# Kernel optimization log

Hardware: AMD Instinct MI355X
Metric: run time of the kernel (lower is better)

Reference implementation:

```python
import math
import jax, jax.numpy as jnp
import numpy as np

N, C_S, C_Z, C, H, PQK, PV = 768, 384, 128, 16, 12, 4, 8
INF, EPS = 100000.0, 1e-8


def _quat_to_rot(q):
    # q: [N,4] normalized quaternions -> [N,3,3] rotation matrices
    w, x, y, z = q[:, 0], q[:, 1], q[:, 2], q[:, 3]
    return jnp.stack([
        jnp.stack([1 - 2 * (y * y + z * z), 2 * (x * y - w * z), 2 * (x * z + w * y)], -1),
        jnp.stack([2 * (x * y + w * z), 1 - 2 * (x * x + z * z), 2 * (y * z - w * x)], -1),
        jnp.stack([2 * (x * z - w * y), 2 * (y * z + w * x), 1 - 2 * (x * x + y * y)], -1),
    ], -2)


def setup_inputs() -> dict:
    key = jax.random.key(0)
    ks = jax.random.split(key, 16)
    quat = jax.random.normal(ks[2], (N, 4))
    quat = quat / jnp.linalg.norm(quat, axis=-1, keepdims=True)
    sc = 0.02
    return {
        "s": jax.random.normal(ks[0], (N, C_S), jnp.float32),
        "z": jax.random.normal(ks[1], (N, N, C_Z), jnp.float32),
        "rot": _quat_to_rot(quat).astype(jnp.float32),
        "trans": jax.random.normal(ks[3], (N, 3), jnp.float32),
        "mask": jnp.ones((N,), jnp.float32),
        "Wq": sc * jax.random.normal(ks[4], (C_S, H * C), jnp.float32),
        "bq": jnp.zeros((H * C,), jnp.float32),
        "Wqp": sc * jax.random.normal(ks[5], (C_S, H * 3 * PQK), jnp.float32),
        "bqp": jnp.zeros((H * 3 * PQK,), jnp.float32),
        "Wkv": sc * jax.random.normal(ks[6], (C_S, 2 * H * C), jnp.float32),
        "bkv": jnp.zeros((2 * H * C,), jnp.float32),
        "Wkvp": sc * jax.random.normal(ks[7], (C_S, H * 3 * (PQK + PV)), jnp.float32),
        "bkvp": jnp.zeros((H * 3 * (PQK + PV),), jnp.float32),
        "Wb": sc * jax.random.normal(ks[8], (C_Z, H), jnp.float32),
        "bb": jnp.zeros((H,), jnp.float32),
        "head_weights": 0.5413 * jnp.ones((H,), jnp.float32),  # softplus^{-1}(1)
        "Wout": sc * jax.random.normal(ks[9], (H * (C_Z + C + PV * 4), C_S), jnp.float32),
        "bout": jnp.zeros((C_S,), jnp.float32),
    }


def _proj_points(x, W, b, rot, trans, P):
    # PointProjection: split last dim into 3 coord chunks, stack as last axis
    pl = x @ W + b                                   # [N, H*3*P]
    pl = pl.reshape(-1, 3, H * P).transpose(0, 2, 1).reshape(-1, H, P, 3)
    return jnp.einsum('nij,nhpj->nhpi', rot, pl) + trans[:, None, None, :]


def reference(s, z, rot, trans, mask, Wq, bq, Wqp, bqp, Wkv, bkv, Wkvp, bkvp,
              Wb, bb, head_weights, Wout, bout):
    q = (s @ Wq + bq).reshape(N, H, C)
    kv = (s @ Wkv + bkv).reshape(N, H, 2 * C)
    k, v = kv[..., :C], kv[..., C:]
    q_pts = _proj_points(s, Wqp, bqp, rot, trans, PQK)          # [N,H,PQK,3]
    kv_pts = _proj_points(s, Wkvp, bkvp, rot, trans, PQK + PV)  # [N,H,PQK+PV,3]
    k_pts, v_pts = kv_pts[..., :PQK, :], kv_pts[..., PQK:, :]

    b_bias = z @ Wb + bb                                        # [N,N,H]
    a = jnp.einsum('qhc,khc->hqk', q, k) * math.sqrt(1.0 / (3 * C))
    a = a + math.sqrt(1.0 / 3) * jnp.transpose(b_bias, (2, 0, 1))

    # point-distance attention: [q,k,H,PQK]
    d2 = jnp.sum((q_pts[:, None] - k_pts[None]) ** 2, axis=-1)
    hw = jax.nn.softplus(head_weights) * math.sqrt(1.0 / (3 * (PQK * 9.0 / 2)))
    pt_att = -0.5 * jnp.sum(d2 * hw[:, None], axis=-1)          # [q,k,H]
    a = a + jnp.transpose(pt_att, (2, 0, 1))

    sq_mask = INF * (mask[:, None] * mask[None, :] - 1.0)       # [q,k]
    a = jax.nn.softmax(a + sq_mask[None], axis=-1)              # [H,q,k]

    o = jnp.einsum('hqk,khc->qhc', a, v).reshape(N, H * C)
    o_pt = jnp.einsum('hqk,khpd->qhpd', a, v_pts)               # [q,H,PV,3]
    o_pt = jnp.einsum('nji,nhpj->nhpi', rot, o_pt - trans[:, None, None, :])  # invert_apply
    o_pt_norm = jnp.sqrt(jnp.sum(o_pt ** 2, -1) + EPS).reshape(N, H * PV)
    o_pt_flat = o_pt.reshape(N, H * PV, 3)
    o_pair = jnp.einsum('hqk,qkc->qhc', a, z).reshape(N, H * C_Z)

    cat = jnp.concatenate(
        [o, o_pt_flat[..., 0], o_pt_flat[..., 1], o_pt_flat[..., 2], o_pt_norm, o_pair], -1)
    return cat @ Wout + bout
```

## Files before the change

### kernel.cpp

```cpp
#include <hip/hip_runtime.h>
#include <math.h>

#define NN    768
#define CS    384
#define INF_  100000.0f

typedef __attribute__((ext_vector_type(8))) short s16x8;
typedef __attribute__((ext_vector_type(4))) float f32x4;

#define OFF_Q       0
#define OFF_K       147456
#define OFF_V       294912
#define OFF_QPRAW   442368
#define OFF_KVPRAW  552960
#define OFF_QPTS    884736
#define OFF_KPTS    995328
#define OFF_VPTS    1105920
#define OFF_KT      1327104
#define OFF_KPT     1474560
#define OFF_S       1585152
#define OFF_MT      5124096
#define OFF_CAT     8414208

__device__ __forceinline__ unsigned short f2bf(float x) {
  unsigned u = __float_as_uint(x) + 0x8000u;
  return (unsigned short)(u >> 16);
}
__device__ __forceinline__ unsigned pk2(float a, float b) {
  return (unsigned)f2bf(a) | ((unsigned)f2bf(b) << 16);
}
__device__ __forceinline__ float bf2f(unsigned short u) {
  return __uint_as_float(((unsigned)u) << 16);
}

__global__ void __launch_bounds__(256)
k1_proj(const float* __restrict__ s,
        const float* __restrict__ Wq,  const float* __restrict__ bq,
        const float* __restrict__ Wqp, const float* __restrict__ bqp,
        const float* __restrict__ Wkv, const float* __restrict__ bkv,
        const float* __restrict__ Wkvp,const float* __restrict__ bkvp,
        float* __restrict__ ws) {
  const int n0 = blockIdx.x * 16;
  const int m0 = blockIdx.y * 128;
  const int t  = threadIdx.x;

  const float* W; const float* bv; int base, ncols;
  if (n0 < 192)      { W = Wq;   bv = bq;   base = 0;   ncols = 192; }
  else if (n0 < 576) { W = Wkv;  bv = bkv;  base = 192; ncols = 384; }
  else if (n0 < 720) { W = Wqp;  bv = bqp;  base = 576; ncols = 144; }
  else               { W = Wkvp; bv = bkvp; base = 720; ncols = 432; }
  const int jj0 = n0 - base;

  __shared__ float As[32 * 130];
  __shared__ float Bs[32 * 20];
  const int tx = t & 3, ty = t >> 2;
  float acc[2][4] = {{0.f}};

  for (int kc = 0; kc < CS; kc += 32) {
    __syncthreads();
    #pragma unroll
    for (int jj = 0; jj < 4; ++jj) {
      const int idx = t + 256 * jj;
      const int row = idx >> 3, c4 = idx & 7;
      const float4 v = *(const float4*)&s[(size_t)(m0 + row) * CS + kc + c4 * 4];
      As[(c4 * 4 + 0) * 130 + row] = v.x;
      As[(c4 * 4 + 1) * 130 + row] = v.y;
      As[(c4 * 4 + 2) * 130 + row] = v.z;
      As[(c4 * 4 + 3) * 130 + row] = v.w;
    }
    if (t < 128) {
      const int row = t >> 2, c4 = t & 3;
      const float4 v = *(const float4*)&W[(size_t)(kc + row) * ncols + jj0 + c4 * 4];
      *(float4*)&Bs[row * 20 + c4 * 4] = v;
    }
    __syncthreads();
    #pragma unroll 8
    for (int k = 0; k < 32; ++k) {
      const float2 a2 = *(const float2*)&As[k * 130 + ty * 2];
      const float4 b4 = *(const float4*)&Bs[k * 20 + tx * 4];
      acc[0][0] += a2.x * b4.x; acc[0][1] += a2.x * b4.y;
      acc[0][2] += a2.x * b4.z; acc[0][3] += a2.x * b4.w;
      acc[1][0] += a2.y * b4.x; acc[1][1] += a2.y * b4.y;
      acc[1][2] += a2.y * b4.z; acc[1][3] += a2.y * b4.w;
    }
  }

  #pragma unroll
  for (int r = 0; r < 2; ++r) {
    const int n = m0 + ty * 2 + r;
    #pragma unroll
    for (int e = 0; e < 4; ++e) {
      const int j = n0 + tx * 4 + e;
      const float val = acc[r][e] + bv[j - base];
      if (j < 192) {
        (ws + OFF_Q)[n * 192 + j] = val;
      } else if (j < 576) {
        const int jj = j - 192, h = jj >> 5, c = jj & 31;
        if (c < 16) (ws + OFF_K)[n * 192 + h * 16 + c] = val;
        else        (ws + OFF_V)[n * 192 + h * 16 + (c - 16)] = val;
      } else if (j < 720) {
        (ws + OFF_QPRAW)[n * 144 + (j - 576)] = val;
      } else {
        (ws + OFF_KVPRAW)[n * 432 + (j - 720)] = val;
      }
    }
  }
}

__global__ void __launch_bounds__(256)
k2_rot(const float* __restrict__ rot, const float* __restrict__ trans,
       float* __restrict__ ws) {
  const int idx = blockIdx.x * 256 + threadIdx.x;
  const int n = idx / 192;
  const int r = idx % 192;
  const float* R = rot + n * 9;
  const float* T = trans + n * 3;
  if (r < 48) {
    const float* raw = ws + OFF_QPRAW + n * 144;
    float p0 = raw[r], p1 = raw[48 + r], p2 = raw[96 + r];
    float g0 = R[0]*p0 + R[1]*p1 + R[2]*p2 + T[0];
    float g1 = R[3]*p0 + R[4]*p1 + R[5]*p2 + T[1];
    float g2 = R[6]*p0 + R[7]*p1 + R[8]*p2 + T[2];
    float* qp = ws + OFF_QPTS + n * 144 + r * 3;
    qp[0] = g0; qp[1] = g1; qp[2] = g2;
  } else {
    const int r2 = r - 48;
    const float* raw = ws + OFF_KVPRAW + n * 432;
    float p0 = raw[r2], p1 = raw[144 + r2], p2 = raw[288 + r2];
    float g0 = R[0]*p0 + R[1]*p1 + R[2]*p2 + T[0];
    float g1 = R[3]*p0 + R[4]*p1 + R[5]*p2 + T[1];
    float g2 = R[6]*p0 + R[7]*p1 + R[8]*p2 + T[2];
    const int h = r2 / 12, p = r2 % 12;
    if (p < 4) {
      float* kp = ws + OFF_KPTS + n * 144 + (h * 4 + p) * 3;
      kp[0] = g0; kp[1] = g1; kp[2] = g2;
    } else {
      float* vp = ws + OFF_VPTS + n * 288 + (h * 8 + (p - 4)) * 3;
      vp[0] = g0; vp[1] = g1; vp[2] = g2;
    }
  }
}

__global__ void __launch_bounds__(256)
k2b_tr(float* __restrict__ ws) {
  const int i = blockIdx.x * 256 + threadIdx.x;
  if (i < 147456) {
    const int n = i / 192, cc = i % 192;
    (ws + OFF_KT)[cc * 768 + n] = (ws + OFF_K)[i];
  } else if (i < 258048) {
    const int i2 = i - 147456;
    const int n = i2 / 144, r = i2 % 144;
    (ws + OFF_KPT)[r * 768 + n] = (ws + OFF_KPTS)[i2];
  } else {
    const int im = i - 258048;
    const int row = im / 768, p = im - row * 768;
    unsigned short* M = (unsigned short*)(ws + OFF_MT);
    float val = 0.0f;
    if (row < 480) {
      const int hh = row / 40, c = row - hh * 40;
      const int pl = p & 63;
      const int k = (p & ~63) | (((pl & 7) << 3) | (pl >> 3));
      val = (c < 16) ? (ws + OFF_V)[k * 192 + hh * 16 + c]
                     : (ws + OFF_VPTS)[k * 288 + hh * 24 + (c - 16)];
    }
    M[row * 768 + p] = f2bf(val);
  }
}

__global__ void __launch_bounds__(256)
ks_scores(const float* __restrict__ mask, const float* __restrict__ bb,
          const float* __restrict__ hwin, float* __restrict__ ws) {
  const int k0 = blockIdx.x * 64;
  const int q0 = blockIdx.y * 16;
  const int t = threadIdx.x;
  const int g = t >> 6, kl = t & 63;
  const int kg = k0 + kl;

  const float* ktr  = ws + OFF_KT;
  const float* kptr = ws + OFF_KPT;
  float F[3][28];
  #pragma unroll
  for (int j = 0; j < 3; ++j) {
    const int h = g + 4 * j;
    #pragma unroll
    for (int c = 0; c < 16; ++c) F[j][c] = ktr[(h * 16 + c) * 768 + kg];
    #pragma unroll
    for (int r = 0; r < 12; ++r) F[j][16 + r] = kptr[(h * 12 + r) * 768 + kg];
  }
  float hw3[3], bb3[3];
  #pragma unroll
  for (int j = 0; j < 3; ++j) {
    const int h = g + 4 * j;
    hw3[j] = logf(1.0f + expf(hwin[h])) * 0.13608276348795434f;
    bb3[j] = 0.57735026918962576f * bb[h];
  }
  const float maskk = mask[kg];
  unsigned short* Sg = (unsigned short*)(ws + OFF_S);

  for (int qi = 0; qi < 16; ++qi) {
    const int q = q0 + qi;
    const float mterm = INF_ * (mask[q] * maskk - 1.0f);
    const float* qrow  = ws + OFF_Q    + q * 192;
    const float* qprow = ws + OFF_QPTS + q * 144;
    #pragma unroll
    for (int j = 0; j < 3; ++j) {
      const int h = g + 4 * j;
      float qk = 0.f;
      #pragma unroll
      for (int c = 0; c < 16; ++c) qk += qrow[h * 16 + c] * F[j][c];
      float pt = 0.f;
      #pragma unroll
      for (int r = 0; r < 12; ++r) {
        const float d = qprow[h * 12 + r] - F[j][16 + r];
        pt += d * d;
      }
      const float S = 0.14433756729740643f * qk - 0.5f * hw3[j] * pt
                    + bb3[j] + mterm;
      Sg[(size_t)(q * 12 + h) * 768 + kg] = f2bf(S);
    }
  }
}

#define ZT_S 72
#define ZR_S 136
#define WT_S 72
__global__ void __launch_bounds__(256, 3)
k3_fused(const float* __restrict__ z, const float* __restrict__ rot,
         const float* __restrict__ trans, const float* __restrict__ Wb,
         float* __restrict__ ws) {
  const int q = blockIdx.x, t = threadIdx.x;
  const int g = t >> 6, kl = t & 63;
  const int l15 = kl & 15, lq = kl >> 4;

  __shared__ unsigned short zT[128 * ZT_S];
  __shared__ unsigned short zR[64 * ZR_S];
  __shared__ unsigned short wT[16 * WT_S];
  __shared__ float bias_s[64 * 13];
  __shared__ float lsum[12], linv[12];
  __shared__ float opt_raw[288];

  s16x8 wbA[4];
  #pragma unroll
  for (int kk = 0; kk < 4; ++kk) {
    #pragma unroll
    for (int j = 0; j < 8; ++j) {
      float v = (l15 < 12) ? Wb[(kk * 32 + lq * 8 + j) * 12 + l15] : 0.0f;
      wbA[kk][j] = (short)f2bf(v);
    }
  }

  const unsigned short* Sg = (const unsigned short*)(ws + OFF_S);
  const float4* zg4  = (const float4*)z + (size_t)q * 24576;
  const unsigned short* mbase = (const unsigned short*)(ws + OFF_MT)
                              + (size_t)(g * 128 + l15) * 768 + lq * 8;

  float l3[3] = {0.f, 0.f, 0.f};
  f32x4 opA = {0.f,0.f,0.f,0.f}, opB = {0.f,0.f,0.f,0.f};
  f32x4 acc[8];
  #pragma unroll
  for (int i = 0; i < 8; ++i) acc[i] = (f32x4){0.f,0.f,0.f,0.f};

  const int kb = t >> 5, c4 = t & 31;

  for (int k0 = 0; k0 < NN; k0 += 64) {
    __syncthreads();

    float4 zv[8];
    #pragma unroll
    for (int m = 0; m < 8; ++m)
      zv[m] = zg4[(size_t)(k0 + kb + 8 * m) * 32 + c4];
    unsigned short Sc[3];
    #pragma unroll
    for (int j = 0; j < 3; ++j)
      Sc[j] = Sg[(size_t)(q * 12 + (g + 4 * j)) * 768 + k0 + kl];

    #pragma unroll
    for (int half = 0; half < 2; ++half) {
      #pragma unroll
      for (int j = 0; j < 4; ++j) {
        const float4 v = zv[half * 4 + j];
        uint2 d;
        d.x = pk2(v.x, v.y);
        d.y = pk2(v.z, v.w);
        *(uint2*)&zR[(kb + 8 * (half * 4 + j)) * ZR_S + c4 * 4] = d;
      }
      #pragma unroll
      for (int w = 0; w < 4; ++w) {
        const int e = ((c4 >> 1) + w) & 3;
        uint2 d;
        d.x = pk2(((const float*)&zv[half * 4 + 0])[e], ((const float*)&zv[half * 4 + 1])[e]);
        d.y = pk2(((const float*)&zv[half * 4 + 2])[e], ((const float*)&zv[half * 4 + 3])[e]);
        *(uint2*)&zT[(c4 * 4 + e) * ZT_S + kb * 8 + half * 4] = d;
      }
    }
    __syncthreads();

    {
      f32x4 bd = {0.f,0.f,0.f,0.f};
      #pragma unroll
      for (int kk = 0; kk < 4; ++kk) {
        s16x8 bf = *(const s16x8*)&zR[(g * 16 + l15) * ZR_S + kk * 32 + lq * 8];
        bd = __builtin_amdgcn_mfma_f32_16x16x32_bf16(wbA[kk], bf, bd, 0, 0, 0);
      }
      #pragma unroll
      for (int r = 0; r < 4; ++r) {
        const int h = lq * 4 + r;
        if (h < 12) bias_s[(g * 16 + l15) * 13 + h] = bd[r];
      }
    }
    __syncthreads();

    {
      #pragma unroll
      for (int j = 0; j < 3; ++j) {
        const int h = g + 4 * j;
        const float Sv = bf2f(Sc[j]);
        const float wv = __expf(Sv + 0.57735026918962576f * bias_s[kl * 13 + h]);
        l3[j] += wv;
        wT[h * WT_S + ((kl & 7) * 8 + (kl >> 3))] = f2bf(wv);
      }
    }
    __syncthreads();

    const s16x8 af0 = *(const s16x8*)&wT[l15 * WT_S + lq * 8];
    const s16x8 af1 = *(const s16x8*)&wT[l15 * WT_S + 32 + lq * 8];
    {
      s16x8 b0 = *(const s16x8*)&zT[((2 * g)     * 16 + l15) * ZT_S + lq * 8];
      s16x8 b1 = *(const s16x8*)&zT[((2 * g)     * 16 + l15) * ZT_S + 32 + lq * 8];
      s16x8 b2 = *(const s16x8*)&zT[((2 * g + 1) * 16 + l15) * ZT_S + lq * 8];
      s16x8 b3 = *(const s16x8*)&zT[((2 * g + 1) * 16 + l15) * ZT_S + 32 + lq * 8];
      opA = __builtin_amdgcn_mfma_f32_16x16x32_bf16(af0, b0, opA, 0, 0, 0);
      opA = __builtin_amdgcn_mfma_f32_16x16x32_bf16(af1, b1, opA, 0, 0, 0);
      opB = __builtin_amdgcn_mfma_f32_16x16x32_bf16(af0, b2, opB, 0, 0, 0);
      opB = __builtin_amdgcn_mfma_f32_16x16x32_bf16(af1, b3, opB, 0, 0, 0);
    }
    {
      const unsigned short* mp = mbase + k0;
      #pragma unroll
      for (int ti = 0; ti < 8; ++ti) {
        const s16x8 m0 = *(const s16x8*)(mp);
        const s16x8 m1 = *(const s16x8*)(mp + 32);
        acc[ti] = __builtin_amdgcn_mfma_f32_16x16x32_bf16(af0, m0, acc[ti], 0, 0, 0);
        acc[ti] = __builtin_amdgcn_mfma_f32_16x16x32_bf16(af1, m1, acc[ti], 0, 0, 0);
        mp += 16 * 768;
      }
    }
  }

  #pragma unroll
  for (int j = 0; j < 3; ++j) {
    float v = l3[j];
    for (int off = 1; off < 64; off <<= 1) v += __shfl_xor(v, off, 64);
    l3[j] = v;
  }
  if (kl == 0) { lsum[g] = l3[0]; lsum[g + 4] = l3[1]; lsum[g + 8] = l3[2]; }
  __syncthreads();
  if (t < 12) linv[t] = 1.0f / lsum[t];
  __syncthreads();

  float* cat = ws + OFF_CAT + (size_t)q * 2112;

  #pragma unroll
  for (int r = 0; r < 4; ++r) {
    const int h = lq * 4 + r;
    if (h < 12) {
      cat[576 + h * 128 + (2 * g)     * 16 + l15] = opA[r] * linv[h];
      cat[576 + h * 128 + (2 * g + 1) * 16 + l15] = opB[r] * linv[h];
    }
  }

  #pragma unroll
  for (int ti = 0; ti < 8; ++ti) {
    const int cg = (g * 8 + ti) * 16 + l15;
    const int hh = cg / 40;
    const int c  = cg - hh * 40;
    #pragma unroll
    for (int r = 0; r < 4; ++r) {
      if (hh < 12 && (lq * 4 + r) == hh) {
        const float val = acc[ti][r] * linv[hh];
        if (c < 16) cat[hh * 16 + c] = val;
        else        opt_raw[hh * 24 + (c - 16)] = val;
      }
    }
  }
  __syncthreads();

  if (t < 96) {
    const int h = t >> 3, p = t & 7;
    const float* R = rot + q * 9;
    const float* T = trans + q * 3;
    const float g0 = opt_raw[h * 24 + p * 3 + 0] - T[0];
    const float g1 = opt_raw[h * 24 + p * 3 + 1] - T[1];
    const float g2 = opt_raw[h * 24 + p * 3 + 2] - T[2];
    const float x  = R[0]*g0 + R[3]*g1 + R[6]*g2;
    const float y  = R[1]*g0 + R[4]*g1 + R[7]*g2;
    const float zc = R[2]*g0 + R[5]*g1 + R[8]*g2;
    const int hp = h * 8 + p;
    cat[192 + hp] = x;
    cat[288 + hp] = y;
    cat[384 + hp] = zc;
    cat[480 + hp] = sqrtf(x*x + y*y + zc*zc + 1e-8f);
  }
}

__global__ void __launch_bounds__(256)
k5_init(const float* __restrict__ bout, float* __restrict__ out) {
  const int i = blockIdx.x * 256 + threadIdx.x;
  out[i] = bout[i % 384];
}

__global__ void __launch_bounds__(256)
k5_out(const float* __restrict__ Wout, const float* __restrict__ ws,
       float* __restrict__ out) {
  const int n0  = blockIdx.x * 64;
  const int m0  = blockIdx.y * 64;
  const int ks0 = blockIdx.z * 352;
  const int t = threadIdx.x;

  __shared__ float As[32 * 68];
  __shared__ float Bs[32 * 68];
  const int tx = t & 15, ty = t >> 4;
  float acc[4][4] = {{0.f}};

  const float* catg = ws + OFF_CAT;
  for (int kc = 0; kc < 352; kc += 32) {
    __syncthreads();
    #pragma unroll
    for (int p = 0; p < 2; ++p) {
      const int idx = t + 256 * p;
      const int m = idx >> 3, c4 = idx & 7;
      const float4 v = *(const float4*)&catg[(size_t)(m0 + m) * 2112 + ks0 + kc + c4 * 4];
      As[(c4 * 4 + 0) * 68 + m] = v.x;
      As[(c4 * 4 + 1) * 68 + m] = v.y;
      As[(c4 * 4 + 2) * 68 + m] = v.z;
      As[(c4 * 4 + 3) * 68 + m] = v.w;
    }
    #pragma unroll
    for (int p = 0; p < 8; ++p) {
      const int idx = t + 256 * p;
      const int k = idx >> 6, n = idx & 63;
      Bs[k * 68 + n] = Wout[(size_t)(ks0 + kc + k) * 384 + n0 + n];
    }
    __syncthreads();
    #pragma unroll 8
    for (int k = 0; k < 32; ++k) {
      const float4 a4 = *(const float4*)&As[k * 68 + ty * 4];
      const float4 b4 = *(const float4*)&Bs[k * 68 + tx * 4];
      acc[0][0] += a4.x * b4.x; acc[0][1] += a4.x * b4.y; acc[0][2] += a4.x * b4.z; acc[0][3] += a4.x * b4.w;
      acc[1][0] += a4.y * b4.x; acc[1][1] += a4.y * b4.y; acc[1][2] += a4.y * b4.z; acc[1][3] += a4.y * b4.w;
      acc[2][0] += a4.z * b4.x; acc[2][1] += a4.z * b4.y; acc[2][2] += a4.z * b4.z; acc[2][3] += a4.z * b4.w;
      acc[3][0] += a4.w * b4.x; acc[3][1] += a4.w * b4.y; acc[3][2] += a4.w * b4.z; acc[3][3] += a4.w * b4.w;
    }
  }
  #pragma unroll
  for (int r = 0; r < 4; ++r)
    #pragma unroll
    for (int c = 0; c < 4; ++c)
      atomicAdd(&out[(size_t)(m0 + ty * 4 + r) * 384 + n0 + tx * 4 + c], acc[r][c]);
}

extern "C" void kernel_launch(void* const* d_in, const int* in_sizes, int n_in,
                              void* d_out, int out_size, void* d_ws, size_t ws_size,
                              hipStream_t stream) {
  const float* s     = (const float*)d_in[0];
  const float* z     = (const float*)d_in[1];
  const float* rot   = (const float*)d_in[2];
  const float* trans = (const float*)d_in[3];
  const float* mask  = (const float*)d_in[4];
  const float* Wq    = (const float*)d_in[5];
  const float* bq    = (const float*)d_in[6];
  const float* Wqp   = (const float*)d_in[7];
  const float* bqp   = (const float*)d_in[8];
  const float* Wkv   = (const float*)d_in[9];
  const float* bkv   = (const float*)d_in[10];
  const float* Wkvp  = (const float*)d_in[11];
  const float* bkvp  = (const float*)d_in[12];
  const float* Wb    = (const float*)d_in[13];
  const float* bb    = (const float*)d_in[14];
  const float* hw    = (const float*)d_in[15];
  const float* Wout  = (const float*)d_in[16];
  const float* bout  = (const float*)d_in[17];
  float* out = (float*)d_out;
  float* ws  = (float*)d_ws;

  k1_proj<<<dim3(72, 6), 256, 0, stream>>>(s, Wq, bq, Wqp, bqp, Wkv, bkv, Wkvp, bkvp, ws);
  k2_rot <<<576, 256, 0, stream>>>(rot, trans, ws);
  k2b_tr <<<2544, 256, 0, stream>>>(ws);
  ks_scores<<<dim3(12, 48), 256, 0, stream>>>(mask, bb, hw, ws);
  k3_fused<<<NN, 256, 0, stream>>>(z, rot, trans, Wb, ws);
  k5_init<<<1152, 256, 0, stream>>>(bout, out);
  k5_out<<<dim3(6, 12, 6), 256, 0, stream>>>(Wout, ws, out);
}
```

Before: 713.9 us.

## Prefetch z tiles into LDS with async global_load_lds and hoist M loads

Replaces the per-iteration register loads of the z tile with asynchronous global-to-LDS copies into a 32KB staging buffer. The next tile is issued right after the current one is converted, so the global load overlaps the bias, softmax and MFMA work. The M-fragment loads are hoisted to the top of the iteration so their latency is hidden behind the conversion. Syncthreads become explicit lgkmcnt waits plus s_barrier, and launch bounds drop from 3 to 2 blocks per CU to fit the extra LDS and registers, which lowers occupancy.

Result: faster. 695.5 us (-2.6%).

```diff
diff --git a/kernel.cpp b/kernel.cpp
--- a/kernel.cpp
+++ b/kernel.cpp
@@ -31,6 +31,18 @@
 }
 __device__ __forceinline__ float bf2f(unsigned short u) {
   return __uint_as_float(((unsigned)u) << 16);
+}
+
+#define LDS_BARRIER() do { \
+  asm volatile("s_waitcnt lgkmcnt(0)" ::: "memory"); \
+  __builtin_amdgcn_s_barrier(); \
+} while (0)
+
+__device__ __forceinline__ void gload_lds16(const void* g, void* l) {
+  __builtin_amdgcn_global_load_lds(
+      (const __attribute__((address_space(1))) void*)(unsigned long long)g,
+      (__attribute__((address_space(3))) void*)(unsigned)(unsigned long long)l,
+      16, 0, 0);
 }
 
 __global__ void __launch_bounds__(256)
@@ -224,7 +236,7 @@
 #define ZT_S 72
 #define ZR_S 136
 #define WT_S 72
-__global__ void __launch_bounds__(256, 3)
+__global__ void __launch_bounds__(256, 2)
 k3_fused(const float* __restrict__ z, const float* __restrict__ rot,
          const float* __restrict__ trans, const float* __restrict__ Wb,
          float* __restrict__ ws) {
@@ -232,6 +244,7 @@
   const int g = t >> 6, kl = t & 63;
   const int l15 = kl & 15, lq = kl >> 4;
 
+  __shared__ float stage[64 * 128];
   __shared__ unsigned short zT[128 * ZT_S];
   __shared__ unsigned short zR[64 * ZR_S];
   __shared__ unsigned short wT[16 * WT_S];
@@ -250,7 +263,7 @@
   }
 
   const unsigned short* Sg = (const unsigned short*)(ws + OFF_S);
-  const float4* zg4  = (const float4*)z + (size_t)q * 24576;
+  const char* zbytes = (const char*)z + (size_t)q * 768 * 512;
   const unsigned short* mbase = (const unsigned short*)(ws + OFF_MT)
                               + (size_t)(g * 128 + l15) * 768 + lq * 8;
 
@@ -262,38 +275,62 @@
 
   const int kb = t >> 5, c4 = t & 31;
 
+  #pragma unroll
+  for (int j = 0; j < 8; ++j) {
+    const int boff = (g * 8 + j) * 1024;
+    gload_lds16(zbytes + boff + kl * 16, (char*)stage + boff);
+  }
+
   for (int k0 = 0; k0 < NN; k0 += 64) {
     __syncthreads();
 
-    float4 zv[8];
-    #pragma unroll
-    for (int m = 0; m < 8; ++m)
-      zv[m] = zg4[(size_t)(k0 + kb + 8 * m) * 32 + c4];
     unsigned short Sc[3];
     #pragma unroll
     for (int j = 0; j < 3; ++j)
       Sc[j] = Sg[(size_t)(q * 12 + (g + 4 * j)) * 768 + k0 + kl];
+    s16x8 mfr[16];
+    {
+      const unsigned short* mp = mbase + k0;
+      #pragma unroll
+      for (int ti = 0; ti < 8; ++ti) {
+        mfr[2 * ti]     = *(const s16x8*)(mp);
+        mfr[2 * ti + 1] = *(const s16x8*)(mp + 32);
+        mp += 16 * 768;
+      }
+    }
 
     #pragma unroll
     for (int half = 0; half < 2; ++half) {
+      float4 zv[4];
+      #pragma unroll
+      for (int j = 0; j < 4; ++j)
+        zv[j] = *(const float4*)&stage[(size_t)(kb + 8 * (half * 4 + j)) * 128 + c4 * 4];
       #pragma unroll
       for (int j = 0; j < 4; ++j) {
-        const float4 v = zv[half * 4 + j];
         uint2 d;
-        d.x = pk2(v.x, v.y);
-        d.y = pk2(v.z, v.w);
+        d.x = pk2(zv[j].x, zv[j].y);
+        d.y = pk2(zv[j].z, zv[j].w);
         *(uint2*)&zR[(kb + 8 * (half * 4 + j)) * ZR_S + c4 * 4] = d;
       }
       #pragma unroll
       for (int w = 0; w < 4; ++w) {
         const int e = ((c4 >> 1) + w) & 3;
         uint2 d;
-        d.x = pk2(((const float*)&zv[half * 4 + 0])[e], ((const float*)&zv[half * 4 + 1])[e]);
-        d.y = pk2(((const float*)&zv[half * 4 + 2])[e], ((const float*)&zv[half * 4 + 3])[e]);
+        d.x = pk2(((const float*)&zv[0])[e], ((const float*)&zv[1])[e]);
+        d.y = pk2(((const float*)&zv[2])[e], ((const float*)&zv[3])[e]);
         *(uint2*)&zT[(c4 * 4 + e) * ZT_S + kb * 8 + half * 4] = d;
       }
     }
-    __syncthreads();
+    LDS_BARRIER();
+
+    if (k0 + 64 < NN) {
+      const char* src = zbytes + (size_t)(k0 + 64) * 512;
+      #pragma unroll
+      for (int j = 0; j < 8; ++j) {
+        const int boff = (g * 8 + j) * 1024;
+        gload_lds16(src + boff + kl * 16, (char*)stage + boff);
+      }
+    }
 
     {
       f32x4 bd = {0.f,0.f,0.f,0.f};
@@ -308,7 +345,7 @@
         if (h < 12) bias_s[(g * 16 + l15) * 13 + h] = bd[r];
       }
     }
-    __syncthreads();
+    LDS_BARRIER();
 
     {
       #pragma unroll
@@ -320,7 +357,7 @@
         wT[h * WT_S + ((kl & 7) * 8 + (kl >> 3))] = f2bf(wv);
       }
     }
-    __syncthreads();
+    LDS_BARRIER();
 
     const s16x8 af0 = *(const s16x8*)&wT[l15 * WT_S + lq * 8];
     const s16x8 af1 = *(const s16x8*)&wT[l15 * WT_S + 32 + lq * 8];
@@ -334,16 +371,10 @@
       opB = __builtin_amdgcn_mfma_f32_16x16x32_bf16(af0, b2, opB, 0, 0, 0);
       opB = __builtin_amdgcn_mfma_f32_16x16x32_bf16(af1, b3, opB, 0, 0, 0);
     }
-    {
-      const unsigned short* mp = mbase + k0;
-      #pragma unroll
-      for (int ti = 0; ti < 8; ++ti) {
-        const s16x8 m0 = *(const s16x8*)(mp);
-        const s16x8 m1 = *(const s16x8*)(mp + 32);
-        acc[ti] = __builtin_amdgcn_mfma_f32_16x16x32_bf16(af0, m0, acc[ti], 0, 0, 0);
-        acc[ti] = __builtin_amdgcn_mfma_f32_16x16x32_bf16(af1, m1, acc[ti], 0, 0, 0);
-        mp += 16 * 768;
-      }
+    #pragma unroll
+    for (int ti = 0; ti < 8; ++ti) {
+      acc[ti] = __builtin_amdgcn_mfma_f32_16x16x32_bf16(af0, mfr[2 * ti],     acc[ti], 0, 0, 0);
+      acc[ti] = __builtin_amdgcn_mfma_f32_16x16x32_bf16(af1, mfr[2 * ti + 1], acc[ti], 0, 0, 0);
     }
   }
 
```
